# Kernel optimization log

Measured on AMD Instinct MI355X. Metric: run time of the kernel, lower is better.

The kernel has to match this reference:

```python
import jax, jax.numpy as jnp
import numpy as np

N_NODES = 100000
N_EDGES = 640000
D_FEAT = 128
UNITS = 128


def setup_inputs() -> dict:
    key = jax.random.key(0)
    k1, k2, k3, k4, k5 = jax.random.split(key, 5)
    X = jax.random.normal(k1, (N_NODES, D_FEAT), dtype=jnp.float32)
    ref_A = jax.random.randint(k2, (N_EDGES,), 0, N_NODES, dtype=jnp.int32)
    ref_B = jax.random.randint(k3, (N_EDGES,), 0, N_NODES, dtype=jnp.int32)
    # GlorotUniform-style params (scale approximated; exact init irrelevant for math)
    limit_w = np.sqrt(6.0 / (D_FEAT + UNITS)).astype(np.float32)
    w = jax.random.uniform(k4, (D_FEAT, UNITS), minval=-limit_w, maxval=limit_w, dtype=jnp.float32)
    b = jax.random.uniform(k5, (UNITS,), minval=-0.1, maxval=0.1, dtype=jnp.float32)
    return {"X": X, "ref_A": ref_A, "ref_B": ref_B, "w": w, "b": b}


def reference(X, ref_A, ref_B, w, b):
    # c.convolution: gather source-node features along edges, scatter-add to
    # destination nodes (sum aggregation over incoming messages).
    msgs = X[ref_A]                                        # [E, D]
    agg = jax.ops.segment_sum(msgs, ref_B, num_segments=X.shape[0])  # [N, D]
    out = agg @ w + b                                      # [N, units]
    return out
```

## Files before the change

kernel.cpp:

```cpp
#include <hip/hip_runtime.h>
#include <hip/hip_bf16.h>

typedef short s16x8 __attribute__((ext_vector_type(8)));
typedef float f32x4 __attribute__((ext_vector_type(4)));

#define CAPN 32

static __device__ inline unsigned short f2bf(float f) {
    __hip_bfloat16 h = __float2bfloat16(f);
    return *reinterpret_cast<unsigned short*>(&h);
}
static __device__ inline float bf2f(unsigned short u) {
    return __uint_as_float((unsigned int)u << 16);
}

__global__ __launch_bounds__(256) void zwt_kernel(
    const float* __restrict__ w, unsigned short* __restrict__ wTh,
    unsigned short* __restrict__ wTl, int* __restrict__ cnt, int Ncap)
{
    int i = blockIdx.x * 256 + threadIdx.x;
    if (i < Ncap) cnt[i] = 0;
    if (i < 16384) {
        int n = i >> 7, k = i & 127;
        float v = w[k * 128 + n];
        unsigned short hi = f2bf(v);
        wTh[i] = hi;
        wTl[i] = f2bf(v - bf2f(hi));
    }
}

__global__ __launch_bounds__(256) void gb_kernel(
    const float* __restrict__ X, const int* __restrict__ A,
    const int* __restrict__ B, const unsigned short* __restrict__ wTh,
    const unsigned short* __restrict__ wTl, int* __restrict__ cnt,
    unsigned int* __restrict__ entries, unsigned short* __restrict__ Yh,
    int N, int E, int EB)
{
    const int tid = threadIdx.x;

    if (blockIdx.x < EB) {
        int i = blockIdx.x * 256 + tid;
        if (i < E) {
            int a = A[i], d = B[i];
            int pos = atomicAdd(&cnt[d], 1);
            if (pos < CAPN)
                entries[(size_t)d * CAPN + pos] = (unsigned int)a;
        }
        return;
    }

    const int gbid = blockIdx.x - EB;
    const int u    = tid >> 6;
    const int lane = tid & 63;
    const int m    = lane & 15;
    const int q    = lane >> 4;
    const int r0   = gbid * 64;
    const int row  = r0 + u * 16 + m;
    const int rldr = (row < N) ? row : (N - 1);

    f32x4 acc[8] = {};
    #pragma unroll
    for (int s = 0; s < 4; ++s) {
        const float* xr = X + (size_t)rldr * 128 + s * 32 + q * 8;
        float4 x0 = *(const float4*)xr;
        float4 x1 = *(const float4*)(xr + 4);
        float xv[8] = {x0.x, x0.y, x0.z, x0.w, x1.x, x1.y, x1.z, x1.w};
        s16x8 ahi, alo;
        #pragma unroll
        for (int j = 0; j < 8; ++j) {
            unsigned short h = f2bf(xv[j]);
            ahi[j] = (short)h;
            alo[j] = (short)f2bf(xv[j] - bf2f(h));
        }
        #pragma unroll
        for (int c = 0; c < 8; ++c) {
            const size_t wo = (size_t)(c * 16 + m) * 128 + s * 32 + q * 8;
            s16x8 bh = *(const s16x8*)&wTh[wo];
            s16x8 bl = *(const s16x8*)&wTl[wo];
            acc[c] = __builtin_amdgcn_mfma_f32_16x16x32_bf16(ahi, bh, acc[c], 0, 0, 0);
            acc[c] = __builtin_amdgcn_mfma_f32_16x16x32_bf16(alo, bh, acc[c], 0, 0, 0);
            acc[c] = __builtin_amdgcn_mfma_f32_16x16x32_bf16(ahi, bl, acc[c], 0, 0, 0);
        }
    }
    const int r0g = r0 + u * 16 + q * 4;
    #pragma unroll
    for (int c = 0; c < 8; ++c) {
        int col = c * 16 + m;
        #pragma unroll
        for (int r = 0; r < 4; ++r) {
            int orow = r0g + r;
            if (orow < N)
                Yh[(size_t)orow * 128 + col] = f2bf(acc[c][r]);
        }
    }
}

__global__ __launch_bounds__(256) void gather_kernel(
    const int* __restrict__ cnt, const unsigned int* __restrict__ entries,
    const unsigned short* __restrict__ Yh, const float* __restrict__ b,
    float* __restrict__ out, int N)
{
    const int tid  = threadIdx.x;
    const int u    = tid >> 6;
    const int lane = tid & 63;
    const int nodeBase = blockIdx.x * 16 + u * 4;

    int deg[4];
    {
        int4 d4 = ((const int4*)cnt)[blockIdx.x * 4 + u];
        deg[0] = d4.x; deg[1] = d4.y; deg[2] = d4.z; deg[3] = d4.w;
    }
    int idxl[4], last[4];
    #pragma unroll
    for (int t = 0; t < 4; ++t) {
        int node = nodeBase + t;
        int dg = (node < N) ? min(deg[t], CAPN) : 0;
        deg[t] = dg;
        last[t] = (dg > 0) ? dg - 1 : 0;
        idxl[t] = (lane < dg) ? (int)entries[(size_t)node * CAPN + lane] : 0;
    }

    const int maxdg = max(max(deg[0], deg[1]), max(deg[2], deg[3]));
    const int maxch = (maxdg + 7) >> 3;
    float ax[4] = {0.f, 0.f, 0.f, 0.f};
    float ay[4] = {0.f, 0.f, 0.f, 0.f};
    #pragma unroll 1
    for (int ch = 0; ch < maxch; ++ch) {
        const int base = ch * 8;
        unsigned int p[4][8];
        #pragma unroll
        for (int t = 0; t < 4; ++t) {
            #pragma unroll
            for (int j = 0; j < 8; ++j) {
                int sl = base + j;
                if (sl > last[t]) sl = last[t];
                int s = __shfl(idxl[t], sl);
                p[t][j] = *(const unsigned int*)(Yh + (size_t)s * 128 + lane * 2);
            }
        }
        #pragma unroll
        for (int t = 0; t < 4; ++t) {
            #pragma unroll
            for (int j = 0; j < 8; ++j)
                if (base + j < deg[t]) {
                    ax[t] += __uint_as_float(p[t][j] << 16);
                    ay[t] += __uint_as_float(p[t][j] & 0xFFFF0000u);
                }
        }
    }

    const float2 bb = ((const float2*)b)[lane];
    #pragma unroll
    for (int t = 0; t < 4; ++t) {
        int node = nodeBase + t;
        if (node < N) {
            float2 o = {ax[t] + bb.x, ay[t] + bb.y};
            ((float2*)(out + (size_t)node * 128))[lane] = o;
        }
    }
}

extern "C" void kernel_launch(void* const* d_in, const int* in_sizes, int n_in,
                              void* d_out, int out_size, void* d_ws, size_t ws_size,
                              hipStream_t stream) {
    const float* X = (const float*)d_in[0];
    const int*   A = (const int*)d_in[1];
    const int*   B = (const int*)d_in[2];
    const float* w = (const float*)d_in[3];
    const float* b = (const float*)d_in[4];
    float* out = (float*)d_out;

    const int N = in_sizes[0] / 128;
    const int E = in_sizes[1];
    const int Ncap = (N + 15) & ~15;

    char* wsb = (char*)d_ws;
    size_t off = 0;
    int* cnt = (int*)(wsb + off); off += (size_t)4 * Ncap;
    off = (off + 255) & ~(size_t)255;
    unsigned short* wTh = (unsigned short*)(wsb + off); off += 32768;
    unsigned short* wTl = (unsigned short*)(wsb + off); off += 32768;
    unsigned int* entries = (unsigned int*)(wsb + off); off += (size_t)N * CAPN * 4;
    off = (off + 255) & ~(size_t)255;
    unsigned short* Yh = (unsigned short*)(wsb + off);

    const int zItems = (Ncap > 16384) ? Ncap : 16384;
    zwt_kernel<<<(zItems + 255) / 256, 256, 0, stream>>>(w, wTh, wTl, cnt, Ncap);

    const int EB = (E + 255) / 256;
    const int GB = (N + 63) / 64;
    gb_kernel<<<EB + GB, 256, 0, stream>>>(X, A, B, wTh, wTl, cnt, entries, Yh, N, E, EB);

    gather_kernel<<<(N + 15) / 16, 256, 0, stream>>>(cnt, entries, Yh, b, out, N);
}
```

Measured before the change: 231.7 us.

## Fuse edge binning into every GEMM block instead of separate edge blocks

Edge binning no longer runs in its own group of blocks. Each GEMM block now loads two edges' indices up front, computes its 64-row X·W tile, and then performs the atomic binning for those edges. A grid-stride loop covers any edges left over. The aim is to hide edge index loads and atomic latency behind the MFMA work and to cut the total block count. The cost is that atomics now sit on the tail of every GEMM block.

Measured after the change: 217.3 us. -6.2%, faster.

```diff
diff --git a/kernel.cpp b/kernel.cpp
--- a/kernel.cpp
+++ b/kernel.cpp
@@ -29,32 +29,27 @@
     }
 }
 
-__global__ __launch_bounds__(256) void gb_kernel(
+__global__ __launch_bounds__(256) void bingemm_kernel(
     const float* __restrict__ X, const int* __restrict__ A,
     const int* __restrict__ B, const unsigned short* __restrict__ wTh,
     const unsigned short* __restrict__ wTl, int* __restrict__ cnt,
     unsigned int* __restrict__ entries, unsigned short* __restrict__ Yh,
-    int N, int E, int EB)
+    int N, int E)
 {
     const int tid = threadIdx.x;
 
-    if (blockIdx.x < EB) {
-        int i = blockIdx.x * 256 + tid;
-        if (i < E) {
-            int a = A[i], d = B[i];
-            int pos = atomicAdd(&cnt[d], 1);
-            if (pos < CAPN)
-                entries[(size_t)d * CAPN + pos] = (unsigned int)a;
-        }
-        return;
-    }
-
-    const int gbid = blockIdx.x - EB;
+    const int e0 = blockIdx.x * 512 + tid;
+    const int e1 = e0 + 256;
+    const bool v0 = (e0 < E), v1 = (e1 < E);
+    int a0 = 0, d0 = 0, a1 = 0, d1 = 0;
+    if (v0) { a0 = A[e0]; d0 = B[e0]; }
+    if (v1) { a1 = A[e1]; d1 = B[e1]; }
+
     const int u    = tid >> 6;
     const int lane = tid & 63;
     const int m    = lane & 15;
     const int q    = lane >> 4;
-    const int r0   = gbid * 64;
+    const int r0   = blockIdx.x * 64;
     const int row  = r0 + u * 16 + m;
     const int rldr = (row < N) ? row : (N - 1);
 
@@ -82,6 +77,7 @@
             acc[c] = __builtin_amdgcn_mfma_f32_16x16x32_bf16(ahi, bl, acc[c], 0, 0, 0);
         }
     }
+
     const int r0g = r0 + u * 16 + q * 4;
     #pragma unroll
     for (int c = 0; c < 8; ++c) {
@@ -92,6 +88,21 @@
             if (orow < N)
                 Yh[(size_t)orow * 128 + col] = f2bf(acc[c][r]);
         }
+    }
+
+    if (v0) {
+        int p = atomicAdd(&cnt[d0], 1);
+        if (p < CAPN) entries[(size_t)d0 * CAPN + p] = (unsigned int)a0;
+    }
+    if (v1) {
+        int p = atomicAdd(&cnt[d1], 1);
+        if (p < CAPN) entries[(size_t)d1 * CAPN + p] = (unsigned int)a1;
+    }
+    for (int e = gridDim.x * 512 + blockIdx.x * 256 + tid; e < E;
+         e += gridDim.x * 256) {
+        int a = A[e], d = B[e];
+        int p = atomicAdd(&cnt[d], 1);
+        if (p < CAPN) entries[(size_t)d * CAPN + p] = (unsigned int)a;
     }
 }
 
@@ -187,9 +198,8 @@
     const int zItems = (Ncap > 16384) ? Ncap : 16384;
     zwt_kernel<<<(zItems + 255) / 256, 256, 0, stream>>>(w, wTh, wTl, cnt, Ncap);
 
-    const int EB = (E + 255) / 256;
     const int GB = (N + 63) / 64;
-    gb_kernel<<<EB + GB, 256, 0, stream>>>(X, A, B, wTh, wTl, cnt, entries, Yh, N, E, EB);
+    bingemm_kernel<<<GB, 256, 0, stream>>>(X, A, B, wTh, wTl, cnt, entries, Yh, N, E);
 
     gather_kernel<<<(N + 15) / 16, 256, 0, stream>>>(cnt, entries, Yh, b, out, N);
 }
```

## Bucket edges by 64-node destination tiles and aggregate in shared memory

Applied to the files above, without the earlier changes.

Replaces the per-node atomic edge list (fixed cap of 32 entries per node) with a counting sort of edges into 64-node destination buckets. A shared-memory histogram, a per-bucket scan and an ordered scatter fill a packed source/row array. A new gather kernel accumulates each bucket's messages into an LDS tile with shared atomics and writes coalesced float4 output rows. The aim is to drop the global per-node atomics and the padded per-node entry layout, at the cost of two extra launches, shared-atomic contention, and silently losing edges if a bucket exceeds 640 entries.

Result: slower. 653.1 us (+181.9%).

```diff
diff --git a/kernel.cpp b/kernel.cpp
--- a/kernel.cpp
+++ b/kernel.cpp
@@ -4,7 +4,9 @@
 typedef short s16x8 __attribute__((ext_vector_type(8)));
 typedef float f32x4 __attribute__((ext_vector_type(4)));
 
-#define CAPN 32
+#define CAPB 640
+#define SB   64
+#define NBMAX 4096
 
 static __device__ inline unsigned short f2bf(float f) {
     __hip_bfloat16 h = __float2bfloat16(f);
@@ -14,12 +16,15 @@
     return __uint_as_float((unsigned int)u << 16);
 }
 
-__global__ __launch_bounds__(256) void zwt_kernel(
-    const float* __restrict__ w, unsigned short* __restrict__ wTh,
-    unsigned short* __restrict__ wTl, int* __restrict__ cnt, int Ncap)
-{
-    int i = blockIdx.x * 256 + threadIdx.x;
-    if (i < Ncap) cnt[i] = 0;
+__global__ __launch_bounds__(256) void hist_kernel(
+    const float* __restrict__ w, const int* __restrict__ B,
+    unsigned short* __restrict__ wTh, unsigned short* __restrict__ wTl,
+    int* __restrict__ part, int NB, int E, int EPB)
+{
+    __shared__ int hist[NBMAX];
+    const int b = blockIdx.x, tid = threadIdx.x;
+
+    int i = b * 256 + tid;
     if (i < 16384) {
         int n = i >> 7, k = i & 127;
         float v = w[k * 128 + n];
@@ -27,34 +32,66 @@
         wTh[i] = hi;
         wTl[i] = f2bf(v - bf2f(hi));
     }
-}
-
-__global__ __launch_bounds__(256) void gb_kernel(
+
+    for (int g = tid; g < NB; g += 256) hist[g] = 0;
+    __syncthreads();
+    const int e0 = b * EPB, e1 = min(E, e0 + EPB);
+    for (int e = e0 + tid; e < e1; e += 256)
+        atomicAdd(&hist[B[e] >> 6], 1);
+    __syncthreads();
+    for (int g = tid; g < NB; g += 256)
+        part[g * SB + b] = hist[g];
+}
+
+__global__ __launch_bounds__(256) void scan_kernel(
+    const int* __restrict__ part, int* __restrict__ offT,
+    int* __restrict__ tot, int NB)
+{
+    const int g    = blockIdx.x * 4 + (threadIdx.x >> 6);
+    const int lane = threadIdx.x & 63;
+    if (g >= NB) return;
+    int v = part[g * SB + lane];
+    int incl = v;
+    #pragma unroll
+    for (int s = 1; s < 64; s <<= 1) {
+        int t = __shfl_up(incl, s);
+        if (lane >= s) incl += t;
+    }
+    offT[lane * NB + g] = g * CAPB + (incl - v);
+    if (lane == 63) tot[g] = incl;
+}
+
+__global__ __launch_bounds__(256) void gemsc_kernel(
     const float* __restrict__ X, const int* __restrict__ A,
     const int* __restrict__ B, const unsigned short* __restrict__ wTh,
-    const unsigned short* __restrict__ wTl, int* __restrict__ cnt,
-    unsigned int* __restrict__ entries, unsigned short* __restrict__ Yh,
-    int N, int E, int EB)
-{
+    const unsigned short* __restrict__ wTl, const int* __restrict__ offT,
+    unsigned int* __restrict__ packed, unsigned short* __restrict__ Yh,
+    int N, int E, int EPB, int NB)
+{
+    __shared__ int cur[NBMAX];
     const int tid = threadIdx.x;
 
-    if (blockIdx.x < EB) {
-        int i = blockIdx.x * 256 + tid;
-        if (i < E) {
-            int a = A[i], d = B[i];
-            int pos = atomicAdd(&cnt[d], 1);
-            if (pos < CAPN)
-                entries[(size_t)d * CAPN + pos] = (unsigned int)a;
+    if (blockIdx.x < SB) {
+        const int b = blockIdx.x;
+        for (int g = tid; g < NB; g += 256) cur[g] = offT[b * NB + g];
+        __syncthreads();
+        const int e0 = b * EPB, e1 = min(E, e0 + EPB);
+        for (int e = e0 + tid; e < e1; e += 256) {
+            int a = A[e], d = B[e];
+            int g = d >> 6;
+            int pos = atomicAdd(&cur[g], 1);
+            if (pos < (g + 1) * CAPB)
+                packed[pos] = (unsigned int)a | ((unsigned int)(d & 63) << 26);
         }
         return;
     }
 
-    const int gbid = blockIdx.x - EB;
+    const int gb   = blockIdx.x - SB;
     const int u    = tid >> 6;
     const int lane = tid & 63;
     const int m    = lane & 15;
     const int q    = lane >> 4;
-    const int r0   = gbid * 64;
+    const int r0   = gb * 64;
     const int row  = r0 + u * 16 + m;
     const int rldr = (row < N) ? row : (N - 1);
 
@@ -82,80 +119,60 @@
             acc[c] = __builtin_amdgcn_mfma_f32_16x16x32_bf16(ahi, bl, acc[c], 0, 0, 0);
         }
     }
+
     const int r0g = r0 + u * 16 + q * 4;
     #pragma unroll
     for (int c = 0; c < 8; ++c) {
         int col = c * 16 + m;
+        int pos = 2 * (col & 63) + (col >> 6);
         #pragma unroll
         for (int r = 0; r < 4; ++r) {
             int orow = r0g + r;
             if (orow < N)
-                Yh[(size_t)orow * 128 + col] = f2bf(acc[c][r]);
-        }
-    }
-}
-
-__global__ __launch_bounds__(256) void gather_kernel(
-    const int* __restrict__ cnt, const unsigned int* __restrict__ entries,
+                Yh[(size_t)orow * 128 + pos] = f2bf(acc[c][r]);
+        }
+    }
+}
+
+__global__ __launch_bounds__(512) void tile_gather_kernel(
+    const unsigned int* __restrict__ packed, const int* __restrict__ tot,
     const unsigned short* __restrict__ Yh, const float* __restrict__ b,
     float* __restrict__ out, int N)
 {
+    __shared__ float tile[64][129];
+    const int g    = blockIdx.x;
     const int tid  = threadIdx.x;
-    const int u    = tid >> 6;
+    const int wv   = tid >> 6;
     const int lane = tid & 63;
-    const int nodeBase = blockIdx.x * 16 + u * 4;
-
-    int deg[4];
-    {
-        int4 d4 = ((const int4*)cnt)[blockIdx.x * 4 + u];
-        deg[0] = d4.x; deg[1] = d4.y; deg[2] = d4.z; deg[3] = d4.w;
-    }
-    int idxl[4], last[4];
-    #pragma unroll
-    for (int t = 0; t < 4; ++t) {
-        int node = nodeBase + t;
-        int dg = (node < N) ? min(deg[t], CAPN) : 0;
-        deg[t] = dg;
-        last[t] = (dg > 0) ? dg - 1 : 0;
-        idxl[t] = (lane < dg) ? (int)entries[(size_t)node * CAPN + lane] : 0;
-    }
-
-    const int maxdg = max(max(deg[0], deg[1]), max(deg[2], deg[3]));
-    const int maxch = (maxdg + 7) >> 3;
-    float ax[4] = {0.f, 0.f, 0.f, 0.f};
-    float ay[4] = {0.f, 0.f, 0.f, 0.f};
-    #pragma unroll 1
-    for (int ch = 0; ch < maxch; ++ch) {
-        const int base = ch * 8;
-        unsigned int p[4][8];
-        #pragma unroll
-        for (int t = 0; t < 4; ++t) {
-            #pragma unroll
-            for (int j = 0; j < 8; ++j) {
-                int sl = base + j;
-                if (sl > last[t]) sl = last[t];
-                int s = __shfl(idxl[t], sl);
-                p[t][j] = *(const unsigned int*)(Yh + (size_t)s * 128 + lane * 2);
-            }
-        }
-        #pragma unroll
-        for (int t = 0; t < 4; ++t) {
-            #pragma unroll
-            for (int j = 0; j < 8; ++j)
-                if (base + j < deg[t]) {
-                    ax[t] += __uint_as_float(p[t][j] << 16);
-                    ay[t] += __uint_as_float(p[t][j] & 0xFFFF0000u);
-                }
-        }
-    }
-
-    const float2 bb = ((const float2*)b)[lane];
-    #pragma unroll
-    for (int t = 0; t < 4; ++t) {
-        int node = nodeBase + t;
-        if (node < N) {
-            float2 o = {ax[t] + bb.x, ay[t] + bb.y};
-            ((float2*)(out + (size_t)node * 128))[lane] = o;
+
+    for (int i = tid; i < 64 * 129; i += 512)
+        (&tile[0][0])[i] = 0.f;
+    __syncthreads();
+
+    const int nseg = min(tot[g], CAPB);
+    const unsigned int* seg = packed + (size_t)g * CAPB;
+    #pragma unroll 2
+    for (int e = wv; e < nseg; e += 8) {
+        unsigned int val = seg[e];
+        int a = val & 0x03FFFFFF;
+        int r = val >> 26;
+        unsigned int yv = *(const unsigned int*)(Yh + (size_t)a * 128 + lane * 2);
+        atomicAdd(&tile[r][lane],      __uint_as_float(yv << 16));
+        atomicAdd(&tile[r][lane + 64], __uint_as_float(yv & 0xFFFF0000u));
+    }
+    __syncthreads();
+
+    const int row = tid >> 3;
+    const int cb  = (tid & 7) * 16;
+    const int orow = g * 64 + row;
+    if (orow < N) {
+        #pragma unroll
+        for (int k = 0; k < 4; ++k) {
+            int col = cb + k * 4;
+            float4 b4 = *(const float4*)(b + col);
+            float4 o = { tile[row][col]     + b4.x, tile[row][col + 1] + b4.y,
+                         tile[row][col + 2] + b4.z, tile[row][col + 3] + b4.w };
+            *(float4*)(out + (size_t)orow * 128 + col) = o;
         }
     }
 }
@@ -170,26 +187,25 @@
     const float* b = (const float*)d_in[4];
     float* out = (float*)d_out;
 
-    const int N = in_sizes[0] / 128;
-    const int E = in_sizes[1];
-    const int Ncap = (N + 15) & ~15;
+    const int N   = in_sizes[0] / 128;
+    const int E   = in_sizes[1];
+    const int NB  = (N + 63) >> 6;
+    const int EPB = (E + SB - 1) / SB;
 
     char* wsb = (char*)d_ws;
     size_t off = 0;
-    int* cnt = (int*)(wsb + off); off += (size_t)4 * Ncap;
+    int* part = (int*)(wsb + off); off += (size_t)NB * SB * 4;
+    int* offT = (int*)(wsb + off); off += (size_t)SB * NB * 4;
+    int* tot  = (int*)(wsb + off); off += (size_t)NB * 4;
     off = (off + 255) & ~(size_t)255;
+    unsigned int* packed = (unsigned int*)(wsb + off); off += (size_t)NB * CAPB * 4;
     unsigned short* wTh = (unsigned short*)(wsb + off); off += 32768;
     unsigned short* wTl = (unsigned short*)(wsb + off); off += 32768;
-    unsigned int* entries = (unsigned int*)(wsb + off); off += (size_t)N * CAPN * 4;
-    off = (off + 255) & ~(size_t)255;
-    unsigned short* Yh = (unsigned short*)(wsb + off);
-
-    const int zItems = (Ncap > 16384) ? Ncap : 16384;
-    zwt_kernel<<<(zItems + 255) / 256, 256, 0, stream>>>(w, wTh, wTl, cnt, Ncap);
-
-    const int EB = (E + 255) / 256;
-    const int GB = (N + 63) / 64;
-    gb_kernel<<<EB + GB, 256, 0, stream>>>(X, A, B, wTh, wTl, cnt, entries, Yh, N, E, EB);
-
-    gather_kernel<<<(N + 15) / 16, 256, 0, stream>>>(cnt, entries, Yh, b, out, N);
-}
+    unsigned short* Yh  = (unsigned short*)(wsb + off);
+
+    hist_kernel<<<SB, 256, 0, stream>>>(w, B, wTh, wTl, part, NB, E, EPB);
+    scan_kernel<<<(NB + 3) / 4, 256, 0, stream>>>(part, offT, tot, NB);
+    gemsc_kernel<<<SB + (N + 63) / 64, 256, 0, stream>>>(
+        X, A, B, wTh, wTl, offT, packed, Yh, N, E, EPB, NB);
+    tile_gather_kernel<<<NB, 512, 0, stream>>>(packed, tot, Yh, b, out, N);
+}
```
